# Performance work log

Hardware: AMD Instinct MI355X
Metric: run time of the kernel (lower is better)

Reference implementation:

```python
import jax, jax.numpy as jnp
import numpy as np

NUM_MID = 10   # hard-coded num_mid_nodes in HiPool.__init__
NUM_HIGH = 5   # ceil(10 / 2)


def map_low_to_high(num_low, num_high):
    # eye(num_high) repeat_interleaved by ceil(low/high) rows, truncated to num_low
    # == one-hot of i // edges_per_high
    edges_per_high = -(-num_low // num_high)
    return jax.nn.one_hot(jnp.arange(num_low) // edges_per_high, num_high,
                          dtype=jnp.float32)  # [low, high]


def cluster_attention(x, mapping, att):
    # x: [s, d], mapping: [s, m], att: [d, d]
    mid = mapping.T @ x                              # [m, d]
    scores = (mid @ att) @ x.T                       # [m, s]
    scores = scores * (1.0 - mapping).T              # zero (not -inf) own-cluster entries, as in source
    scores = jax.nn.softmax(scores, axis=1)
    return scores @ x + mid                          # [m, d]


def dense_gcn(x, adj, W, b):
    # torch_geometric DenseGCNConv with add_loop=True
    n = adj.shape[0]
    i = jnp.arange(n)
    adj = adj.at[i, i].set(1.0)
    deg = jnp.clip(jnp.sum(adj, axis=-1), 1.0, None) ** -0.5
    adj = deg[:, None] * adj * deg[None, :]
    return adj @ (x @ W) + b


def setup_inputs() -> dict:
    key = jax.random.key(0)
    ks = jax.random.split(key, 8)
    S, D, H = 8192, 768, 768
    return {
        "x": jax.random.normal(ks[0], (S, D), dtype=jnp.float32),
        "adjacency_matrix": jax.random.uniform(ks[1], (S, S), dtype=jnp.float32),
        "att_low_mid": jax.random.normal(ks[2], (D, D), dtype=jnp.float32) * 0.04,  # xavier_normal-ish
        "conv1_w": jax.random.normal(ks[3], (D, H), dtype=jnp.float32) * 0.04,
        "conv1_b": jnp.zeros((H,), dtype=jnp.float32),
        "att_mid_high": jax.random.normal(ks[4], (H, H), dtype=jnp.float32) * 0.04,
        "conv2_w": jax.random.normal(ks[5], (H, H), dtype=jnp.float32) * 0.04,
        "conv2_b": jnp.zeros((H,), dtype=jnp.float32),
    }


def reference(x, adjacency_matrix, att_low_mid, conv1_w, conv1_b,
              att_mid_high, conv2_w, conv2_b):
    s = x.shape[0]
    m1 = map_low_to_high(s, NUM_MID)                         # [s, 10]
    mid_adj = m1.T @ adjacency_matrix @ m1                   # [10, 10]
    mid_rep = cluster_attention(x, m1, att_low_mid)          # [10, d]
    x_mid = jax.nn.relu(dense_gcn(mid_rep, mid_adj, conv1_w, conv1_b))
    # F.dropout(...)[0]: dropout treated as identity (eval); [0] just dropped the batch dim
    m2 = map_low_to_high(NUM_MID, NUM_HIGH)                  # [10, 5]
    high_adj = m2.T @ mid_adj @ m2                           # [5, 5]
    high_rep = cluster_attention(x_mid, m2, att_mid_high)    # [5, h]
    out = jax.nn.relu(dense_gcn(high_rep, high_adj, conv2_w, conv2_b))
    return out.mean(axis=0)                                  # [h]
```

## Files before the change

### kernel.cpp

```cpp
#include <hip/hip_runtime.h>

constexpr int S    = 8192;
constexpr int D    = 768;
constexpr int NMID = 10;
constexpr int EPH  = 820;

constexpr int PART_ADJ = 0;
constexpr int PART_MID = 3200;
constexpr int OFF_ZB   = 64640;
constexpr int OFF_MATT = 64640;
constexpr int OFF_Y1   = 72320;
constexpr int OFF_Z2   = 80000;
constexpr int OFF_Y2   = 83840;
constexpr int ZERO_N   = 23040;
constexpr int OFF_MID  = 87680;
constexpr int OFF_XMID = 95360;
constexpr int OFF_SC   = 103040;
constexpr int OFF_SCB  = 184960;
constexpr int OFF_PVP  = 190080;

__device__ __forceinline__ void adj_partial(const float* __restrict__ A,
                                            float* __restrict__ ws, int item) {
    __shared__ float wred[4];
    int p = item >> 5, s = item & 31;
    int i = p / 10, j = p % 10;
    int r0 = i * EPH, nr = min(EPH, S - r0);
    int c0 = j * EPH, nc = min(EPH, S - c0);
    int rs0 = r0 + (nr * s) / 32, rs1 = r0 + (nr * (s + 1)) / 32;
    int nc4 = nc >> 2;
    int tid = threadIdx.x;
    float acc = 0.f;
    for (int r = rs0; r < rs1; ++r) {
        const float4* row = (const float4*)(A + (size_t)r * S + c0);
        if (tid < nc4) {
            float4 v = row[tid];
            acc += (v.x + v.y) + (v.z + v.w);
        }
    }
#pragma unroll
    for (int off = 32; off > 0; off >>= 1) acc += __shfl_down(acc, off, 64);
    int ln = tid & 63, wv = tid >> 6;
    if (ln == 0) wred[wv] = acc;
    __syncthreads();
    if (tid == 0) ws[PART_ADJ + item] = (wred[0] + wred[1]) + (wred[2] + wred[3]);
}

__device__ __forceinline__ void mid_partial(const float* __restrict__ x,
                                            float* __restrict__ ws, int item) {
    int cl = item / 24, rem = item % 24;
    int cc = rem >> 3, sp = rem & 7;
    int r0 = cl * EPH, nr = min(EPH, S - r0);
    int rs0 = r0 + (nr * sp) / 8, rs1 = r0 + (nr * (sp + 1)) / 8;
    int c = cc * 256 + threadIdx.x;
    float acc = 0.f;
    for (int r = rs0; r < rs1; ++r) acc += x[(size_t)r * D + c];
    ws[PART_MID + (sp * NMID + cl) * D + c] = acc;
}

template <int NR>
__device__ __forceinline__ void mm_core(const float* __restrict__ W,
                                        const float* mi,
                                        float* __restrict__ out, int kb) {
    int c = threadIdx.x;
    float a0[NR], a1[NR], a2[NR];
#pragma unroll
    for (int i = 0; i < NR; ++i) { a0[i] = 0.f; a1[i] = 0.f; a2[i] = 0.f; }
    for (int kk = 0; kk < 16; ++kk) {
        const float* wr = W + (size_t)(kb + kk) * D;
        float w0 = wr[c], w1 = wr[c + 256], w2 = wr[c + 512];
#pragma unroll
        for (int i = 0; i < NR; ++i) {
            float m = mi[i * 16 + kk];
            a0[i] += m * w0; a1[i] += m * w1; a2[i] += m * w2;
        }
    }
#pragma unroll
    for (int i = 0; i < NR; ++i) {
        atomicAdd(&out[i * D + c],       a0[i]);
        atomicAdd(&out[i * D + c + 256], a1[i]);
        atomicAdd(&out[i * D + c + 512], a2[i]);
    }
}

__global__ __launch_bounds__(256) void k1(const float* __restrict__ A,
                                          const float* __restrict__ x,
                                          float* __restrict__ ws) {
    int bx = blockIdx.x;
    if (bx < 800) adj_partial(A, ws, bx);
    else if (bx < 1040) mid_partial(x, ws, bx - 800);
    else {
        int b = bx - 1040;
        for (int t = b * 256 + threadIdx.x; t < ZERO_N; t += 16 * 256)
            ws[OFF_ZB + t] = 0.f;
    }
}

__global__ __launch_bounds__(256) void k2(const float* __restrict__ attL,
                                          const float* __restrict__ A,
                                          float* __restrict__ ws) {
    int bx = blockIdx.x;
    if (bx >= 48) { adj_partial(A, ws, 800 + bx - 48); return; }
    __shared__ float mi[160];
    int kb = bx * 16, tid = threadIdx.x;
    if (tid < 160) {
        int cl = tid >> 4, k = tid & 15;
        float s = 0.f;
#pragma unroll
        for (int sp = 0; sp < 8; ++sp)
            s += ws[PART_MID + (sp * NMID + cl) * D + kb + k];
        mi[tid] = s;
        ws[OFF_MID + cl * D + kb + k] = s;
    }
    __syncthreads();
    mm_core<10>(attL, mi, ws + OFF_MATT, kb);
}

__global__ __launch_bounds__(256) void k3(const float* __restrict__ x,
                                          const float* __restrict__ A,
                                          float* __restrict__ ws) {
    int bx = blockIdx.x;
    if (bx >= 256) { adj_partial(A, ws, 1600 + bx - 256); return; }
    __shared__ float ma[NMID * D];
    __shared__ float scl[32 * NMID];
    int tid = threadIdx.x;
    for (int t = tid; t < NMID * D; t += 256) ma[t] = ws[OFF_MATT + t];
    __syncthreads();
    const float4* maf = (const float4*)ma;
    const float4* x4  = (const float4*)x;
    int wave = tid >> 6, ln = tid & 63;
    int rbase = bx * 32 + wave * 8;
    for (int rr = 0; rr < 8; ++rr) {
        int r = rbase + rr;
        float4 v0 = x4[(size_t)r * 192 + ln];
        float4 v1 = x4[(size_t)r * 192 + 64 + ln];
        float4 v2 = x4[(size_t)r * 192 + 128 + ln];
        int rc = r / EPH;
#pragma unroll
        for (int i = 0; i < NMID; ++i) {
            float4 m0 = maf[i * 192 + ln];
            float4 m1 = maf[i * 192 + 64 + ln];
            float4 m2 = maf[i * 192 + 128 + ln];
            float p = m0.x * v0.x + m0.y * v0.y + m0.z * v0.z + m0.w * v0.w
                    + m1.x * v1.x + m1.y * v1.y + m1.z * v1.z + m1.w * v1.w
                    + m2.x * v2.x + m2.y * v2.y + m2.z * v2.z + m2.w * v2.w;
#pragma unroll
            for (int off = 32; off > 0; off >>= 1) p += __shfl_down(p, off, 64);
            if (ln == 0) {
                float v = (rc == i) ? 0.f : p;
                ws[OFF_SC + r * NMID + i] = v;
                scl[(wave * 8 + rr) * NMID + i] = v;
            }
        }
    }
    __syncthreads();
    if (tid < NMID) {
        float m = -1e30f;
        for (int r = 0; r < 32; ++r) m = fmaxf(m, scl[r * NMID + tid]);
        float s = 0.f;
        for (int r = 0; r < 32; ++r) s += expf(scl[r * NMID + tid] - m);
        ws[OFF_SCB + bx * 20 + tid * 2]     = m;
        ws[OFF_SCB + bx * 20 + tid * 2 + 1] = s;
    }
}

__global__ __launch_bounds__(256) void k4(const float* __restrict__ x,
                                          const float* __restrict__ A,
                                          float* __restrict__ ws) {
    int bx = blockIdx.x;
    if (bx >= 64) { adj_partial(A, ws, 2200 + bx - 64); return; }
    __shared__ float lm[160], ls[160], Mi[10], Inv[10], p[128 * NMID];
    int tid = threadIdx.x;
    if (tid < 160) {
        int i = tid >> 4, seg = tid & 15;
        float m = -1e30f;
        for (int b = seg * 16; b < seg * 16 + 16; ++b)
            m = fmaxf(m, ws[OFF_SCB + b * 20 + i * 2]);
        float s = 0.f;
        for (int b = seg * 16; b < seg * 16 + 16; ++b)
            s += ws[OFF_SCB + b * 20 + i * 2 + 1] *
                 expf(ws[OFF_SCB + b * 20 + i * 2] - m);
        lm[tid] = m; ls[tid] = s;
    }
    __syncthreads();
    if (tid < NMID) {
        float M = -1e30f;
        for (int g = 0; g < 16; ++g) M = fmaxf(M, lm[tid * 16 + g]);
        float Ssum = 0.f;
        for (int g = 0; g < 16; ++g) Ssum += ls[tid * 16 + g] * expf(lm[tid * 16 + g] - M);
        Mi[tid] = M; Inv[tid] = 1.f / Ssum;
    }
    __syncthreads();
    int r0 = bx * 128;
    for (int t = tid; t < 128 * NMID; t += 256) {
        int i = t % NMID;
        p[t] = expf(ws[OFF_SC + r0 * NMID + t] - Mi[i]) * Inv[i];
    }
    __syncthreads();
    float a0[NMID], a1[NMID], a2[NMID];
#pragma unroll
    for (int i = 0; i < NMID; ++i) { a0[i] = 0.f; a1[i] = 0.f; a2[i] = 0.f; }
    for (int r = 0; r < 128; ++r) {
        const float* xr = x + (size_t)(r0 + r) * D;
        float x0 = xr[tid], x1 = xr[tid + 256], x2 = xr[tid + 512];
#pragma unroll
        for (int i = 0; i < NMID; ++i) {
            float pv = p[r * NMID + i];
            a0[i] += pv * x0; a1[i] += pv * x1; a2[i] += pv * x2;
        }
    }
#pragma unroll
    for (int i = 0; i < NMID; ++i) {
        float* base = ws + OFF_PVP + (bx * NMID + i) * D;
        base[tid]       = a0[i];
        base[tid + 256] = a1[i];
        base[tid + 512] = a2[i];
    }
}

__global__ __launch_bounds__(256) void k5(const float* __restrict__ W1,
                                          const float* __restrict__ A,
                                          float* __restrict__ ws) {
    int bx = blockIdx.x;
    if (bx >= 48) { adj_partial(A, ws, 2800 + bx - 48); return; }
    __shared__ float mi[160];
    int kb = bx * 16, tid = threadIdx.x;
    if (tid < 160) {
        int cl = tid >> 4, k = tid & 15;
        float s = ws[OFF_MID + cl * D + kb + k];
        for (int b = 0; b < 64; ++b)
            s += ws[OFF_PVP + (b * NMID + cl) * D + kb + k];
        mi[tid] = s;
    }
    __syncthreads();
    mm_core<10>(W1, mi, ws + OFF_Y1, kb);
}

__global__ __launch_bounds__(256) void k6(const float* __restrict__ attH,
                                          const float* __restrict__ b1,
                                          float* __restrict__ ws) {
    __shared__ float aa[100], dg[10], NM[100], xml[160], mi[80];
    int tid = threadIdx.x;
    if (tid < 100) {
        float s = 0.f;
#pragma unroll
        for (int sp = 0; sp < 32; ++sp) s += ws[PART_ADJ + tid * 32 + sp];
        aa[tid] = s;
    }
    __syncthreads();
    if (tid < 10) {
        float s = 0.f;
#pragma unroll
        for (int j = 0; j < 10; ++j) s += (tid == j) ? 1.0f : aa[tid * 10 + j];
        dg[tid] = 1.0f / sqrtf(fmaxf(s, 1.0f));
    }
    __syncthreads();
    if (tid < 100) {
        int i = tid / 10, j = tid % 10;
        NM[tid] = dg[i] * ((i == j) ? 1.0f : aa[tid]) * dg[j];
    }
    __syncthreads();
    int kb = blockIdx.x * 16;
    if (tid < 160) {
        int i = tid >> 4, c = kb + (tid & 15);
        float s = b1[c];
#pragma unroll
        for (int j = 0; j < 10; ++j) s += NM[i * 10 + j] * ws[OFF_Y1 + j * D + c];
        float xm = fmaxf(s, 0.f);
        ws[OFF_XMID + i * D + c] = xm;
        xml[tid] = xm;
    }
    __syncthreads();
    if (tid < 80) {
        int a = tid >> 4, k = tid & 15;
        mi[tid] = xml[(2 * a) * 16 + k] + xml[(2 * a + 1) * 16 + k];
    }
    __syncthreads();
    mm_core<5>(attH, mi, ws + OFF_Z2, kb);
}

__global__ __launch_bounds__(256) void k7(const float* __restrict__ W2,
                                          float* __restrict__ ws) {
    __shared__ float s2[64], P2[50], mi[80];
    int tid = threadIdx.x, wv = tid >> 6, ln = tid & 63;
    for (int pp = wv; pp < 50; pp += 4) {
        int i = pp / 10, r = pp % 10;
        const float4* za = (const float4*)(ws + OFF_Z2 + i * D);
        const float4* xa = (const float4*)(ws + OFF_XMID + r * D);
        float acc = 0.f;
#pragma unroll
        for (int q = 0; q < 3; ++q) {
            float4 a = za[q * 64 + ln], b = xa[q * 64 + ln];
            acc += a.x * b.x + a.y * b.y + a.z * b.z + a.w * b.w;
        }
#pragma unroll
        for (int off = 32; off > 0; off >>= 1) acc += __shfl_down(acc, off, 64);
        if (ln == 0) s2[pp] = ((r >> 1) == i) ? 0.f : acc;
    }
    __syncthreads();
    if (tid < 5) {
        float mx = -1e30f;
#pragma unroll
        for (int r = 0; r < 10; ++r) mx = fmaxf(mx, s2[tid * 10 + r]);
        float sm = 0.f; float e[10];
#pragma unroll
        for (int r = 0; r < 10; ++r) { e[r] = expf(s2[tid * 10 + r] - mx); sm += e[r]; }
#pragma unroll
        for (int r = 0; r < 10; ++r) P2[tid * 10 + r] = e[r] / sm;
    }
    __syncthreads();
    int kb = blockIdx.x * 16;
    if (tid < 80) {
        int i = tid >> 4, c = kb + (tid & 15);
        float xm[10];
#pragma unroll
        for (int r = 0; r < 10; ++r) xm[r] = ws[OFF_XMID + r * D + c];
        float o = xm[2 * i] + xm[2 * i + 1];
#pragma unroll
        for (int r = 0; r < 10; ++r) o += P2[i * 10 + r] * xm[r];
        mi[tid] = o;
    }
    __syncthreads();
    mm_core<5>(W2, mi, ws + OFF_Y2, kb);
}

__global__ __launch_bounds__(768) void k8(const float* __restrict__ b2,
                                          const float* __restrict__ ws,
                                          float* __restrict__ out) {
    __shared__ float aa[100], ha[25], dh[5], NH[25];
    int tid = threadIdx.x;
    if (tid < 100) {
        float s = 0.f;
#pragma unroll
        for (int sp = 0; sp < 32; ++sp) s += ws[PART_ADJ + tid * 32 + sp];
        aa[tid] = s;
    }
    __syncthreads();
    if (tid < 25) {
        int a = tid / 5, b = tid % 5;
        ha[tid] = aa[(2 * a) * 10 + 2 * b] + aa[(2 * a) * 10 + 2 * b + 1]
                + aa[(2 * a + 1) * 10 + 2 * b] + aa[(2 * a + 1) * 10 + 2 * b + 1];
    }
    __syncthreads();
    if (tid < 5) {
        float s = 0.f;
#pragma unroll
        for (int j = 0; j < 5; ++j) s += (tid == j) ? 1.0f : ha[tid * 5 + j];
        dh[tid] = 1.0f / sqrtf(fmaxf(s, 1.0f));
    }
    __syncthreads();
    if (tid < 25) {
        int i = tid / 5, j = tid % 5;
        NH[tid] = dh[i] * ((i == j) ? 1.0f : ha[tid]) * dh[j];
    }
    __syncthreads();
    int c = tid;
    float y[5];
#pragma unroll
    for (int j = 0; j < 5; ++j) y[j] = ws[OFF_Y2 + j * D + c];
    float bias = b2[c];
    float s = 0.f;
#pragma unroll
    for (int i = 0; i < 5; ++i) {
        float v = bias;
#pragma unroll
        for (int j = 0; j < 5; ++j) v += NH[i * 5 + j] * y[j];
        s += fmaxf(v, 0.f);
    }
    out[c] = s * 0.2f;
}

extern "C" void kernel_launch(void* const* d_in, const int* in_sizes, int n_in,
                              void* d_out, int out_size, void* d_ws, size_t ws_size,
                              hipStream_t stream) {
    const float* x    = (const float*)d_in[0];
    const float* adj  = (const float*)d_in[1];
    const float* attL = (const float*)d_in[2];
    const float* W1   = (const float*)d_in[3];
    const float* b1   = (const float*)d_in[4];
    const float* attH = (const float*)d_in[5];
    const float* W2   = (const float*)d_in[6];
    const float* b2   = (const float*)d_in[7];
    float* ws  = (float*)d_ws;
    float* out = (float*)d_out;

    k1<<<1056, 256, 0, stream>>>(adj, x, ws);
    k2<<<848,  256, 0, stream>>>(attL, adj, ws);
    k3<<<856,  256, 0, stream>>>(x, adj, ws);
    k4<<<664,  256, 0, stream>>>(x, adj, ws);
    k5<<<448,  256, 0, stream>>>(W1, adj, ws);
    k6<<<48,   256, 0, stream>>>(attH, b1, ws);
    k7<<<48,   256, 0, stream>>>(W2, ws);
    k8<<<1,    768, 0, stream>>>(b2, ws, out);
}
```

Before: 160.1 us.

## Merge tail kernels into one persistent kernel with grid barriers

Cuts the pipeline from eight launches to four. The softmax-weighted accumulation is folded into the score kernel using local maxima, with the global rescale done later. The GCN and second-level attention stages run in a single 48-block kernel synchronised by software grid barriers. Adjacency partial sums are redistributed across the first three kernels, and the attention and W2 products use full-K slices instead of atomics. This removes launch gaps and atomic traffic, but relies on all 48 blocks being co-resident for the spin barrier.

```diff
diff --git a/kernel.cpp b/kernel.cpp
--- a/kernel.cpp
+++ b/kernel.cpp
@@ -4,20 +4,18 @@
 constexpr int D    = 768;
 constexpr int NMID = 10;
 constexpr int EPH  = 820;
+constexpr int TAILB = 48;
 
 constexpr int PART_ADJ = 0;
 constexpr int PART_MID = 3200;
-constexpr int OFF_ZB   = 64640;
-constexpr int OFF_MATT = 64640;
-constexpr int OFF_Y1   = 72320;
-constexpr int OFF_Z2   = 80000;
-constexpr int OFF_Y2   = 83840;
-constexpr int ZERO_N   = 23040;
-constexpr int OFF_MID  = 87680;
-constexpr int OFF_XMID = 95360;
-constexpr int OFF_SC   = 103040;
-constexpr int OFF_SCB  = 184960;
-constexpr int OFF_PVP  = 190080;
+constexpr int OFF_Y1   = 64640;
+constexpr int OFF_Z2   = 72320;
+constexpr int OFF_MATT = 76160;
+constexpr int OFF_XMID = 83840;
+constexpr int OFF_MID2 = 91520;
+constexpr int OFF_SCB  = 95360;
+constexpr int OFF_PVP  = 97920;
+constexpr int OFF_BAR  = 1081344;
 
 __device__ __forceinline__ void adj_partial(const float* __restrict__ A,
                                             float* __restrict__ ws, int item) {
@@ -82,55 +80,104 @@
     }
 }
 
+template <int NR>
+__device__ __forceinline__ void fullk_slice(const float* __restrict__ W,
+                                            const float* inL, float* red,
+                                            float* outS, int c0) {
+    int tid = threadIdx.x;
+    int c = tid & 15, ks = tid >> 4;
+    float acc[NR];
+#pragma unroll
+    for (int i = 0; i < NR; ++i) acc[i] = 0.f;
+    int kb = ks * 48;
+    for (int kk = 0; kk < 48; ++kk) {
+        int k = kb + kk;
+        float w = W[(size_t)k * D + c0 + c];
+#pragma unroll
+        for (int i = 0; i < NR; ++i) acc[i] += inL[i * D + k] * w;
+    }
+#pragma unroll
+    for (int i = 0; i < NR; ++i) red[(ks * NR + i) * 16 + c] = acc[i];
+    __syncthreads();
+    if (tid < NR * 16) {
+        int i = tid >> 4, cc = tid & 15;
+        float s = 0.f;
+#pragma unroll
+        for (int k2 = 0; k2 < 16; ++k2) s += red[(k2 * NR + i) * 16 + cc];
+        outS[i * 16 + cc] = s;
+    }
+    __syncthreads();
+}
+
+__device__ __forceinline__ void gbar(unsigned* bar) {
+    __syncthreads();
+    if (threadIdx.x == 0) {
+        __threadfence();
+        unsigned g = __hip_atomic_load(bar + 32, __ATOMIC_RELAXED, __HIP_MEMORY_SCOPE_AGENT);
+        unsigned a = __hip_atomic_fetch_add(bar, 1u, __ATOMIC_ACQ_REL, __HIP_MEMORY_SCOPE_AGENT);
+        if (a == (unsigned)(TAILB - 1)) {
+            __hip_atomic_store(bar, 0u, __ATOMIC_RELAXED, __HIP_MEMORY_SCOPE_AGENT);
+            __hip_atomic_fetch_add(bar + 32, 1u, __ATOMIC_RELEASE, __HIP_MEMORY_SCOPE_AGENT);
+        } else {
+            while (__hip_atomic_load(bar + 32, __ATOMIC_ACQUIRE, __HIP_MEMORY_SCOPE_AGENT) == g)
+                __builtin_amdgcn_s_sleep(8);
+        }
+        __threadfence();
+    }
+    __syncthreads();
+}
+
 __global__ __launch_bounds__(256) void k1(const float* __restrict__ A,
                                           const float* __restrict__ x,
                                           float* __restrict__ ws) {
-    int bx = blockIdx.x;
-    if (bx < 800) adj_partial(A, ws, bx);
-    else if (bx < 1040) mid_partial(x, ws, bx - 800);
+    int bx = blockIdx.x, tid = threadIdx.x;
+    if (bx < 1280) adj_partial(A, ws, bx);
+    else if (bx < 1520) mid_partial(x, ws, bx - 1280);
     else {
-        int b = bx - 1040;
-        for (int t = b * 256 + threadIdx.x; t < ZERO_N; t += 16 * 256)
-            ws[OFF_ZB + t] = 0.f;
+        int b = bx - 1520;
+        for (int t = b * 256 + tid; t < 11520; t += 768) ws[OFF_Y1 + t] = 0.f;
+        if (b == 0 && tid < 64) ((unsigned*)(ws + OFF_BAR))[tid] = 0u;
     }
 }
 
 __global__ __launch_bounds__(256) void k2(const float* __restrict__ attL,
                                           const float* __restrict__ A,
                                           float* __restrict__ ws) {
-    int bx = blockIdx.x;
-    if (bx >= 48) { adj_partial(A, ws, 800 + bx - 48); return; }
-    __shared__ float mi[160];
-    int kb = bx * 16, tid = threadIdx.x;
-    if (tid < 160) {
-        int cl = tid >> 4, k = tid & 15;
+    int bx = blockIdx.x, tid = threadIdx.x;
+    if (bx >= 48) { adj_partial(A, ws, 1280 + bx - 48); return; }
+    __shared__ float midL[7680];
+    __shared__ float red[2560];
+    __shared__ float outS[160];
+    for (int t = tid; t < 7680; t += 256) {
+        int cl = t / D, k = t - cl * D;
         float s = 0.f;
 #pragma unroll
         for (int sp = 0; sp < 8; ++sp)
-            s += ws[PART_MID + (sp * NMID + cl) * D + kb + k];
-        mi[tid] = s;
-        ws[OFF_MID + cl * D + kb + k] = s;
-    }
-    __syncthreads();
-    mm_core<10>(attL, mi, ws + OFF_MATT, kb);
+            s += ws[PART_MID + (sp * NMID + cl) * D + k];
+        midL[t] = s;
+    }
+    __syncthreads();
+    fullk_slice<10>(attL, midL, red, outS, bx * 16);
+    if (tid < 160) ws[OFF_MATT + (tid >> 4) * D + bx * 16 + (tid & 15)] = outS[tid];
 }
 
 __global__ __launch_bounds__(256) void k3(const float* __restrict__ x,
                                           const float* __restrict__ A,
                                           float* __restrict__ ws) {
-    int bx = blockIdx.x;
-    if (bx >= 256) { adj_partial(A, ws, 1600 + bx - 256); return; }
-    __shared__ float ma[NMID * D];
-    __shared__ float scl[32 * NMID];
-    int tid = threadIdx.x;
-    for (int t = tid; t < NMID * D; t += 256) ma[t] = ws[OFF_MATT + t];
+    int bx = blockIdx.x, tid = threadIdx.x;
+    if (bx >= 128) { adj_partial(A, ws, 2240 + bx - 128); return; }
+    __shared__ float ma[7680];
+    __shared__ float sl[640];
+    __shared__ float mloc[10];
+    for (int t = tid; t < 7680; t += 256) ma[t] = ws[OFF_MATT + t];
     __syncthreads();
     const float4* maf = (const float4*)ma;
     const float4* x4  = (const float4*)x;
     int wave = tid >> 6, ln = tid & 63;
-    int rbase = bx * 32 + wave * 8;
-    for (int rr = 0; rr < 8; ++rr) {
-        int r = rbase + rr;
+    int r0 = bx * 64;
+    for (int rr = 0; rr < 16; ++rr) {
+        int rl = wave * 16 + rr;
+        int r = r0 + rl;
         float4 v0 = x4[(size_t)r * 192 + ln];
         float4 v1 = x4[(size_t)r * 192 + 64 + ln];
         float4 v2 = x4[(size_t)r * 192 + 128 + ln];
@@ -145,67 +192,32 @@
                     + m2.x * v2.x + m2.y * v2.y + m2.z * v2.z + m2.w * v2.w;
 #pragma unroll
             for (int off = 32; off > 0; off >>= 1) p += __shfl_down(p, off, 64);
-            if (ln == 0) {
-                float v = (rc == i) ? 0.f : p;
-                ws[OFF_SC + r * NMID + i] = v;
-                scl[(wave * 8 + rr) * NMID + i] = v;
-            }
+            if (ln == 0) sl[rl * NMID + i] = (rc == i) ? 0.f : p;
         }
     }
     __syncthreads();
     if (tid < NMID) {
         float m = -1e30f;
-        for (int r = 0; r < 32; ++r) m = fmaxf(m, scl[r * NMID + tid]);
-        float s = 0.f;
-        for (int r = 0; r < 32; ++r) s += expf(scl[r * NMID + tid] - m);
+        for (int r = 0; r < 64; ++r) m = fmaxf(m, sl[r * NMID + tid]);
+        float s = 0.f;
+        for (int r = 0; r < 64; ++r) s += expf(sl[r * NMID + tid] - m);
+        mloc[tid] = m;
         ws[OFF_SCB + bx * 20 + tid * 2]     = m;
         ws[OFF_SCB + bx * 20 + tid * 2 + 1] = s;
     }
-}
-
-__global__ __launch_bounds__(256) void k4(const float* __restrict__ x,
-                                          const float* __restrict__ A,
-                                          float* __restrict__ ws) {
-    int bx = blockIdx.x;
-    if (bx >= 64) { adj_partial(A, ws, 2200 + bx - 64); return; }
-    __shared__ float lm[160], ls[160], Mi[10], Inv[10], p[128 * NMID];
-    int tid = threadIdx.x;
-    if (tid < 160) {
-        int i = tid >> 4, seg = tid & 15;
-        float m = -1e30f;
-        for (int b = seg * 16; b < seg * 16 + 16; ++b)
-            m = fmaxf(m, ws[OFF_SCB + b * 20 + i * 2]);
-        float s = 0.f;
-        for (int b = seg * 16; b < seg * 16 + 16; ++b)
-            s += ws[OFF_SCB + b * 20 + i * 2 + 1] *
-                 expf(ws[OFF_SCB + b * 20 + i * 2] - m);
-        lm[tid] = m; ls[tid] = s;
-    }
-    __syncthreads();
-    if (tid < NMID) {
-        float M = -1e30f;
-        for (int g = 0; g < 16; ++g) M = fmaxf(M, lm[tid * 16 + g]);
-        float Ssum = 0.f;
-        for (int g = 0; g < 16; ++g) Ssum += ls[tid * 16 + g] * expf(lm[tid * 16 + g] - M);
-        Mi[tid] = M; Inv[tid] = 1.f / Ssum;
-    }
-    __syncthreads();
-    int r0 = bx * 128;
-    for (int t = tid; t < 128 * NMID; t += 256) {
-        int i = t % NMID;
-        p[t] = expf(ws[OFF_SC + r0 * NMID + t] - Mi[i]) * Inv[i];
-    }
+    __syncthreads();
+    for (int t = tid; t < 640; t += 256) sl[t] = expf(sl[t] - mloc[t % NMID]);
     __syncthreads();
     float a0[NMID], a1[NMID], a2[NMID];
 #pragma unroll
     for (int i = 0; i < NMID; ++i) { a0[i] = 0.f; a1[i] = 0.f; a2[i] = 0.f; }
-    for (int r = 0; r < 128; ++r) {
+    for (int r = 0; r < 64; ++r) {
         const float* xr = x + (size_t)(r0 + r) * D;
         float x0 = xr[tid], x1 = xr[tid + 256], x2 = xr[tid + 512];
 #pragma unroll
         for (int i = 0; i < NMID; ++i) {
-            float pv = p[r * NMID + i];
-            a0[i] += pv * x0; a1[i] += pv * x1; a2[i] += pv * x2;
+            float w = sl[r * NMID + i];
+            a0[i] += w * x0; a1[i] += w * x1; a2[i] += w * x2;
         }
     }
 #pragma unroll
@@ -217,29 +229,64 @@
     }
 }
 
-__global__ __launch_bounds__(256) void k5(const float* __restrict__ W1,
-                                          const float* __restrict__ A,
-                                          float* __restrict__ ws) {
-    int bx = blockIdx.x;
-    if (bx >= 48) { adj_partial(A, ws, 2800 + bx - 48); return; }
+__global__ __launch_bounds__(256) void k4(const float* __restrict__ W1,
+                                          const float* __restrict__ b1,
+                                          const float* __restrict__ attH,
+                                          const float* __restrict__ W2,
+                                          const float* __restrict__ b2,
+                                          float* __restrict__ ws,
+                                          float* __restrict__ out) {
+    __shared__ float lm[160], ls[160], Mi[16], Zi[16];
+    __shared__ float wts[1280];
     __shared__ float mi[160];
-    int kb = bx * 16, tid = threadIdx.x;
+    __shared__ float aa[100], dg[16], NM[100], xml[160], mi2[80];
+    __shared__ float sred[200], s2l[64], P2[50];
+    __shared__ float out2L[3840], red[1280], Y2s[80];
+    __shared__ float ha[32], dh[8], NH[32];
+    unsigned* bar = (unsigned*)(ws + OFF_BAR);
+    int bx = blockIdx.x, tid = threadIdx.x;
+    int kb = bx * 16;
+
     if (tid < 160) {
-        int cl = tid >> 4, k = tid & 15;
-        float s = ws[OFF_MID + cl * D + kb + k];
-        for (int b = 0; b < 64; ++b)
-            s += ws[OFF_PVP + (b * NMID + cl) * D + kb + k];
+        int i = tid >> 4, seg = tid & 15;
+        float m = -1e30f;
+        for (int b = seg * 8; b < seg * 8 + 8; ++b)
+            m = fmaxf(m, ws[OFF_SCB + b * 20 + i * 2]);
+        float s = 0.f;
+        for (int b = seg * 8; b < seg * 8 + 8; ++b)
+            s += ws[OFF_SCB + b * 20 + i * 2 + 1] *
+                 expf(ws[OFF_SCB + b * 20 + i * 2] - m);
+        lm[tid] = m; ls[tid] = s;
+    }
+    __syncthreads();
+    if (tid < NMID) {
+        float M = -1e30f;
+        for (int g = 0; g < 16; ++g) M = fmaxf(M, lm[tid * 16 + g]);
+        float Z = 0.f;
+        for (int g = 0; g < 16; ++g) Z += ls[tid * 16 + g] * expf(lm[tid * 16 + g] - M);
+        Mi[tid] = M; Zi[tid] = 1.f / Z;
+    }
+    __syncthreads();
+    for (int t = tid; t < 1280; t += 256) {
+        int b = t / NMID, i = t % NMID;
+        wts[t] = expf(ws[OFF_SCB + b * 20 + i * 2] - Mi[i]) * Zi[i];
+    }
+    __syncthreads();
+    if (tid < 160) {
+        int i = tid >> 4, k = kb + (tid & 15);
+        float s = 0.f;
+#pragma unroll
+        for (int sp = 0; sp < 8; ++sp)
+            s += ws[PART_MID + (sp * NMID + i) * D + k];
+        for (int b = 0; b < 128; ++b)
+            s += wts[b * NMID + i] * ws[OFF_PVP + (b * NMID + i) * D + k];
         mi[tid] = s;
     }
     __syncthreads();
     mm_core<10>(W1, mi, ws + OFF_Y1, kb);
-}
-
-__global__ __launch_bounds__(256) void k6(const float* __restrict__ attH,
-                                          const float* __restrict__ b1,
-                                          float* __restrict__ ws) {
-    __shared__ float aa[100], dg[10], NM[100], xml[160], mi[80];
-    int tid = threadIdx.x;
+
+    gbar(bar);
+
     if (tid < 100) {
         float s = 0.f;
 #pragma unroll
@@ -250,91 +297,72 @@
     if (tid < 10) {
         float s = 0.f;
 #pragma unroll
-        for (int j = 0; j < 10; ++j) s += (tid == j) ? 1.0f : aa[tid * 10 + j];
-        dg[tid] = 1.0f / sqrtf(fmaxf(s, 1.0f));
+        for (int j = 0; j < 10; ++j) s += (tid == j) ? 1.f : aa[tid * 10 + j];
+        dg[tid] = 1.f / sqrtf(fmaxf(s, 1.f));
     }
     __syncthreads();
     if (tid < 100) {
         int i = tid / 10, j = tid % 10;
-        NM[tid] = dg[i] * ((i == j) ? 1.0f : aa[tid]) * dg[j];
-    }
-    __syncthreads();
-    int kb = blockIdx.x * 16;
+        NM[tid] = dg[i] * ((i == j) ? 1.f : aa[tid]) * dg[j];
+    }
+    __syncthreads();
     if (tid < 160) {
         int i = tid >> 4, c = kb + (tid & 15);
-        float s = b1[c];
-#pragma unroll
-        for (int j = 0; j < 10; ++j) s += NM[i * 10 + j] * ws[OFF_Y1 + j * D + c];
-        float xm = fmaxf(s, 0.f);
+        float v = b1[c];
+#pragma unroll
+        for (int j = 0; j < 10; ++j) v += NM[i * 10 + j] * ws[OFF_Y1 + j * D + c];
+        float xm = fmaxf(v, 0.f);
         ws[OFF_XMID + i * D + c] = xm;
         xml[tid] = xm;
     }
     __syncthreads();
     if (tid < 80) {
-        int a = tid >> 4, k = tid & 15;
-        mi[tid] = xml[(2 * a) * 16 + k] + xml[(2 * a + 1) * 16 + k];
-    }
-    __syncthreads();
-    mm_core<5>(attH, mi, ws + OFF_Z2, kb);
-}
-
-__global__ __launch_bounds__(256) void k7(const float* __restrict__ W2,
-                                          float* __restrict__ ws) {
-    __shared__ float s2[64], P2[50], mi[80];
-    int tid = threadIdx.x, wv = tid >> 6, ln = tid & 63;
-    for (int pp = wv; pp < 50; pp += 4) {
+        int a = tid >> 4, cc = tid & 15;
+        float m2v = xml[(2 * a) * 16 + cc] + xml[(2 * a + 1) * 16 + cc];
+        ws[OFF_MID2 + a * D + kb + cc] = m2v;
+        mi2[tid] = m2v;
+    }
+    __syncthreads();
+    mm_core<5>(attH, mi2, ws + OFF_Z2, kb);
+
+    gbar(bar);
+
+    if (tid < 200) {
+        int pp = tid >> 2, q = tid & 3;
         int i = pp / 10, r = pp % 10;
-        const float4* za = (const float4*)(ws + OFF_Z2 + i * D);
-        const float4* xa = (const float4*)(ws + OFF_XMID + r * D);
-        float acc = 0.f;
-#pragma unroll
-        for (int q = 0; q < 3; ++q) {
-            float4 a = za[q * 64 + ln], b = xa[q * 64 + ln];
-            acc += a.x * b.x + a.y * b.y + a.z * b.z + a.w * b.w;
-        }
-#pragma unroll
-        for (int off = 32; off > 0; off >>= 1) acc += __shfl_down(acc, off, 64);
-        if (ln == 0) s2[pp] = ((r >> 1) == i) ? 0.f : acc;
+        const float* z  = ws + OFF_Z2 + i * D;
+        const float* xm = ws + OFF_XMID + r * D;
+        float s = 0.f;
+        for (int c = q * 192; c < q * 192 + 192; ++c) s += z[c] * xm[c];
+        sred[tid] = s;
+    }
+    __syncthreads();
+    if (tid < 50) {
+        int i = tid / 10, r = tid % 10;
+        float v = sred[tid * 4] + sred[tid * 4 + 1] + sred[tid * 4 + 2] + sred[tid * 4 + 3];
+        s2l[tid] = ((r >> 1) == i) ? 0.f : v;
     }
     __syncthreads();
     if (tid < 5) {
         float mx = -1e30f;
 #pragma unroll
-        for (int r = 0; r < 10; ++r) mx = fmaxf(mx, s2[tid * 10 + r]);
+        for (int r = 0; r < 10; ++r) mx = fmaxf(mx, s2l[tid * 10 + r]);
         float sm = 0.f; float e[10];
 #pragma unroll
-        for (int r = 0; r < 10; ++r) { e[r] = expf(s2[tid * 10 + r] - mx); sm += e[r]; }
+        for (int r = 0; r < 10; ++r) { e[r] = expf(s2l[tid * 10 + r] - mx); sm += e[r]; }
 #pragma unroll
         for (int r = 0; r < 10; ++r) P2[tid * 10 + r] = e[r] / sm;
     }
     __syncthreads();
-    int kb = blockIdx.x * 16;
-    if (tid < 80) {
-        int i = tid >> 4, c = kb + (tid & 15);
-        float xm[10];
-#pragma unroll
-        for (int r = 0; r < 10; ++r) xm[r] = ws[OFF_XMID + r * D + c];
-        float o = xm[2 * i] + xm[2 * i + 1];
-#pragma unroll
-        for (int r = 0; r < 10; ++r) o += P2[i * 10 + r] * xm[r];
-        mi[tid] = o;
-    }
-    __syncthreads();
-    mm_core<5>(W2, mi, ws + OFF_Y2, kb);
-}
-
-__global__ __launch_bounds__(768) void k8(const float* __restrict__ b2,
-                                          const float* __restrict__ ws,
-                                          float* __restrict__ out) {
-    __shared__ float aa[100], ha[25], dh[5], NH[25];
-    int tid = threadIdx.x;
-    if (tid < 100) {
-        float s = 0.f;
-#pragma unroll
-        for (int sp = 0; sp < 32; ++sp) s += ws[PART_ADJ + tid * 32 + sp];
-        aa[tid] = s;
-    }
-    __syncthreads();
+    for (int t = tid; t < 3840; t += 256) {
+        int i = t / D, k = t - i * D;
+        float v = ws[OFF_MID2 + t];
+#pragma unroll
+        for (int r = 0; r < 10; ++r) v += P2[i * 10 + r] * ws[OFF_XMID + r * D + k];
+        out2L[t] = v;
+    }
+    __syncthreads();
+    fullk_slice<5>(W2, out2L, red, Y2s, kb);
     if (tid < 25) {
         int a = tid / 5, b = tid % 5;
         ha[tid] = aa[(2 * a) * 10 + 2 * b] + aa[(2 * a) * 10 + 2 * b + 1]
@@ -344,29 +372,28 @@
     if (tid < 5) {
         float s = 0.f;
 #pragma unroll
-        for (int j = 0; j < 5; ++j) s += (tid == j) ? 1.0f : ha[tid * 5 + j];
-        dh[tid] = 1.0f / sqrtf(fmaxf(s, 1.0f));
+        for (int j = 0; j < 5; ++j) s += (tid == j) ? 1.f : ha[tid * 5 + j];
+        dh[tid] = 1.f / sqrtf(fmaxf(s, 1.f));
     }
     __syncthreads();
     if (tid < 25) {
         int i = tid / 5, j = tid % 5;
-        NH[tid] = dh[i] * ((i == j) ? 1.0f : ha[tid]) * dh[j];
-    }
-    __syncthreads();
-    int c = tid;
-    float y[5];
-#pragma unroll
-    for (int j = 0; j < 5; ++j) y[j] = ws[OFF_Y2 + j * D + c];
-    float bias = b2[c];
-    float s = 0.f;
-#pragma unroll
-    for (int i = 0; i < 5; ++i) {
-        float v = bias;
-#pragma unroll
-        for (int j = 0; j < 5; ++j) v += NH[i * 5 + j] * y[j];
-        s += fmaxf(v, 0.f);
-    }
-    out[c] = s * 0.2f;
+        NH[tid] = dh[i] * ((i == j) ? 1.f : ha[tid]) * dh[j];
+    }
+    __syncthreads();
+    if (tid < 16) {
+        int c = kb + tid;
+        float bias = b2[c];
+        float s = 0.f;
+#pragma unroll
+        for (int i = 0; i < 5; ++i) {
+            float v = bias;
+#pragma unroll
+            for (int j = 0; j < 5; ++j) v += NH[i * 5 + j] * Y2s[j * 16 + tid];
+            s += fmaxf(v, 0.f);
+        }
+        out[c] = s * 0.2f;
+    }
 }
 
 extern "C" void kernel_launch(void* const* d_in, const int* in_sizes, int n_in,
@@ -383,12 +410,8 @@
     float* ws  = (float*)d_ws;
     float* out = (float*)d_out;
 
-    k1<<<1056, 256, 0, stream>>>(adj, x, ws);
-    k2<<<848,  256, 0, stream>>>(attL, adj, ws);
-    k3<<<856,  256, 0, stream>>>(x, adj, ws);
-    k4<<<664,  256, 0, stream>>>(x, adj, ws);
-    k5<<<448,  256, 0, stream>>>(W1, adj, ws);
-    k6<<<48,   256, 0, stream>>>(attH, b1, ws);
-    k7<<<48,   256, 0, stream>>>(W2, ws);
-    k8<<<1,    768, 0, stream>>>(b2, ws, out);
-}
+    k1<<<1523, 256, 0, stream>>>(adj, x, ws);
+    k2<<<1008, 256, 0, stream>>>(attL, adj, ws);
+    k3<<<1088, 256, 0, stream>>>(x, adj, ws);
+    k4<<<TAILB, 256, 0, stream>>>(W1, b1, attH, W2, b2, ws, out);
+}
```

Result: slower. 177.8 us (+11.0%).
